# Performance work log

Hardware: AMD Instinct MI355X
Metric: run time of the kernel (lower is better)

## Reference

```python
import jax, jax.numpy as jnp
import numpy as np
import math

D_MODEL = 1024
N_HEADS = 16
HEAD_DIM = D_MODEL // N_HEADS
B, T = 2, 2048


def _rope(q, k):
    # q, k: (B, H, T, Dh)
    Dh = q.shape[-1]
    Tq = q.shape[2]
    dim = jnp.arange(0, Dh, 2, dtype=jnp.float32)
    inv_freq = 1.0 / (10000.0 ** (dim / Dh))
    pos = jnp.arange(Tq, dtype=jnp.float32)
    freqs = pos[:, None] * inv_freq[None, :]          # (T, Dh/2)
    sin = jnp.sin(freqs)[None, None]                  # (1,1,T,Dh/2)
    cos = jnp.cos(freqs)[None, None]

    def rot(t):
        te, to = t[..., ::2], t[..., 1::2]
        re = te * cos - to * sin
        ro = te * sin + to * cos
        return jnp.stack([re, ro], axis=-1).reshape(t.shape)

    return rot(q), rot(k)


def setup_inputs() -> dict:
    key = jax.random.key(0)
    ks = jax.random.split(key, 4)
    std = 1.0 / math.sqrt(D_MODEL)
    x = jax.random.normal(ks[0], (B, T, D_MODEL), dtype=jnp.float32)
    W_qkv = jax.random.normal(ks[1], (D_MODEL, 3 * D_MODEL), dtype=jnp.float32) * std
    b_qkv = jnp.zeros((3 * D_MODEL,), dtype=jnp.float32)
    W_out = jax.random.normal(ks[2], (D_MODEL, D_MODEL), dtype=jnp.float32) * std
    b_out = jnp.zeros((D_MODEL,), dtype=jnp.float32)
    attention_mask = jnp.ones((B, T), dtype=jnp.int32)
    return {"x": x, "attention_mask": attention_mask, "W_qkv": W_qkv,
            "b_qkv": b_qkv, "W_out": W_out, "b_out": b_out}


def reference(x, attention_mask, W_qkv, b_qkv, W_out, b_out):
    Bx, Tx, D = x.shape
    qkv = x @ W_qkv + b_qkv                            # (B,T,3D)
    q, k, v = jnp.split(qkv, 3, axis=-1)
    # (B,T,H,Dh) -> (B,H,T,Dh)
    q = q.reshape(Bx, Tx, N_HEADS, HEAD_DIM).transpose(0, 2, 1, 3)
    k = k.reshape(Bx, Tx, N_HEADS, HEAD_DIM).transpose(0, 2, 1, 3)
    v = v.reshape(Bx, Tx, N_HEADS, HEAD_DIM).transpose(0, 2, 1, 3)
    q, k = _rope(q, k)
    scale = 1.0 / math.sqrt(float(HEAD_DIM))
    scores = jnp.einsum('bhqd,bhkd->bhqk', q, k) * scale
    causal = jnp.tril(jnp.ones((Tx, Tx), dtype=bool))[None, None]
    pad = attention_mask.astype(bool)[:, None, None, :]
    mask = causal & pad
    scores = jnp.where(mask, scores, -jnp.inf)
    probs = jax.nn.softmax(scores, axis=-1)
    out = jnp.einsum('bhqk,bhkd->bhqd', probs, v)      # (B,H,T,Dh)
    out = out.transpose(0, 2, 1, 3).reshape(Bx, Tx, D)
    return out @ W_out + b_out
```

## Files before the change

kernel.cpp:

```cpp
#include <hip/hip_runtime.h>
#include <math.h>
#include <stdint.h>

#define D_MODEL 1024
#define N_HEADS 16
#define HEAD_DIM 64
#define BATCH 2
#define SEQ 2048
#define TOKENS (BATCH * SEQ)

typedef __attribute__((ext_vector_type(8))) short short8;
typedef __attribute__((ext_vector_type(8))) _Float16 half8;
typedef __attribute__((ext_vector_type(4))) float floatx4;

#define BMFMA(a, b, c) __builtin_amdgcn_mfma_f32_16x16x32_bf16(a, b, c, 0, 0, 0)
#define HMFMA(a, b, c) __builtin_amdgcn_mfma_f32_16x16x32_f16(a, b, c, 0, 0, 0)

__device__ __forceinline__ unsigned short f2bf(float f) {
    uint32_t u = __float_as_uint(f);
    u += 0x7fffu + ((u >> 16) & 1u);
    return (unsigned short)(u >> 16);
}
__device__ __forceinline__ float bf2f(unsigned short h) {
    return __uint_as_float(((uint32_t)h) << 16);
}
__device__ __forceinline__ unsigned short f2h(float f) {
    union { _Float16 h; unsigned short u; } cv;
    cv.h = (_Float16)f;
    return cv.u;
}
__device__ __forceinline__ float h2f(unsigned short u) {
    union { unsigned short u; _Float16 h; } cv;
    cv.u = u;
    return (float)cv.h;
}

#define GLD_LDS16(gp, lp) __builtin_amdgcn_global_load_lds(                 \
    (const __attribute__((address_space(1))) void*)(gp),                    \
    (__attribute__((address_space(3))) void*)(lp), 16, 0, 0)

__global__ __launch_bounds__(256) void split_inputs(
    const float* __restrict__ X, const float* __restrict__ Wqkv,
    const float* __restrict__ Wout, const int* __restrict__ am,
    unsigned short* __restrict__ Axh, unsigned short* __restrict__ Bt,
    unsigned short* __restrict__ Bt2, unsigned long long* __restrict__ mbits,
    float2* __restrict__ tab)
{
    __shared__ float t[32][33];
    const int tid = threadIdx.x;
    const int bid = blockIdx.x;
    if (bid < 4096) {
        const int idx = bid * 256 + tid;
        const int row = idx >> 8;
        const int c = (idx & 255) * 4;
        float4 v = *(const float4*)(X + (size_t)row * 1024 + c);
        float f[4] = {v.x, v.y, v.z, v.w};
        uint32_t hp[2], lp[2];
#pragma unroll
        for (int j = 0; j < 2; ++j) {
            unsigned short h0 = f2h(f[2 * j]), h1 = f2h(f[2 * j + 1]);
            hp[j] = (uint32_t)h0 | ((uint32_t)h1 << 16);
            lp[j] = (uint32_t)f2h(f[2 * j] - h2f(h0)) |
                    ((uint32_t)f2h(f[2 * j + 1] - h2f(h1)) << 16);
        }
        *(uint2*)(Axh + (size_t)row * 2048 + c) = make_uint2(hp[0], hp[1]);
        *(uint2*)(Axh + (size_t)row * 2048 + 1024 + c) = make_uint2(lp[0], lp[1]);
    } else if (bid < 7168) {
        const int id = bid - 4096;
        const int n0 = (id % 96) * 32, k0 = (id / 96) * 32;
        const int c = tid & 31, r = tid >> 5;
#pragma unroll
        for (int i = 0; i < 4; ++i)
            t[r + 8 * i][c] = Wqkv[(size_t)(k0 + r + 8 * i) * 3072 + n0 + c];
        __syncthreads();
#pragma unroll
        for (int i = 0; i < 4; ++i) {
            int dn = r + 8 * i;
            Bt[(size_t)(n0 + dn) * 1024 + k0 + c] = f2h(t[c][dn]);
        }
    } else if (bid < 8192) {
        const int id = bid - 7168;
        const int n0 = (id & 31) * 32, k0 = (id >> 5) * 32;
        const int c = tid & 31, r = tid >> 5;
#pragma unroll
        for (int i = 0; i < 4; ++i)
            t[r + 8 * i][c] = Wout[(size_t)(k0 + r + 8 * i) * 1024 + n0 + c];
        __syncthreads();
#pragma unroll
        for (int i = 0; i < 4; ++i) {
            int dn = r + 8 * i;
            Bt2[(size_t)(n0 + dn) * 1024 + k0 + c] = f2bf(t[c][dn]);
        }
    } else if (bid == 8192) {
        if (tid < 64) {
            const int* a = am + tid * 64;
            unsigned long long m = 0ull;
            for (int j = 0; j < 64; ++j)
                m |= (unsigned long long)(a[j] != 0 ? 1u : 0u) << j;
            mbits[tid] = m;
        }
    } else {
        const int i = bid - 8193;
#pragma unroll
        for (int e = 0; e < 16; ++e) {
            int idx = i * 4096 + e * 256 + tid;
            int tt = idx >> 5, pr = idx & 31;
            double ex = (double)(2 * pr) / 64.0;
            float inv = (float)exp2(-ex * 13.287712379549449);
            float ang = (float)tt * inv;
            float s, c;
            __sincosf(ang, &s, &c);
            tab[idx] = make_float2(c, s);
        }
    }
}

__global__ __launch_bounds__(256) void gemm_qkv_f16(
    const unsigned short* __restrict__ Axh, const unsigned short* __restrict__ Bt,
    const float* __restrict__ bias, float* __restrict__ C)
{
    __shared__ __align__(16) unsigned short sAh0[4096], sAh1[4096];
    __shared__ __align__(16) unsigned short sAl0[4096], sAl1[4096];
    __shared__ __align__(16) unsigned short sB0[4096],  sB1[4096];

    const int tid = threadIdx.x;
    const int w = tid >> 6, lane = tid & 63;
    const int l15 = lane & 15, quad = lane >> 4;
    const int wm = w >> 1, wn = w & 1;

    const bool qk = blockIdx.x < 512;
    const int lin = qk ? blockIdx.x : blockIdx.x - 512;
    const int nT = qk ? 16 : 8;
    const int msuper = lin / (8 * nT);
    const int rem = lin % (8 * nT);
    const int m0 = (msuper * 8 + (rem & 7)) * 128;
    const int n0 = (qk ? 0 : 2048) + (rem >> 3) * 128;

    const int ch = (lane & 3) ^ ((lane >> 3) & 3);
    const int sw = (quad ^ ((l15 >> 1) & 3)) * 8;

    const unsigned short* aG[2];
    const unsigned short* bG[2];
#pragma unroll
    for (int i = 0; i < 2; ++i) {
        aG[i] = Axh + (size_t)(m0 + (w * 2 + i) * 16 + (lane >> 2)) * 2048
                    + ch * 8;
        bG[i] = Bt + (size_t)(n0 + (w * 2 + i) * 16 + (lane >> 2)) * 1024
                   + ch * 8;
    }

    floatx4 acc[4][4];
#pragma unroll
    for (int fm = 0; fm < 4; ++fm)
#pragma unroll
        for (int fn = 0; fn < 4; ++fn) acc[fm][fn] = (floatx4)0.f;

    for (int ks = 0; ks < 16; ++ks) {
        const int ko = ks * 64;
        __syncthreads();
#pragma unroll
        for (int i = 0; i < 2; ++i) {
            GLD_LDS16(aG[i] + ko,        sAh0 + (w * 2 + i) * 512);
            GLD_LDS16(aG[i] + ko + 32,   sAh1 + (w * 2 + i) * 512);
            GLD_LDS16(bG[i] + ko,        sB0 + (w * 2 + i) * 512);
            GLD_LDS16(bG[i] + ko + 32,   sB1 + (w * 2 + i) * 512);
        }
        if (qk) {
#pragma unroll
            for (int i = 0; i < 2; ++i) {
                GLD_LDS16(aG[i] + 1024 + ko,      sAl0 + (w * 2 + i) * 512);
                GLD_LDS16(aG[i] + 1024 + ko + 32, sAl1 + (w * 2 + i) * 512);
            }
        }
        __syncthreads();

        half8 b0[4], b1[4];
#pragma unroll
        for (int fn = 0; fn < 4; ++fn) {
            const int off = ((wn * 4 + fn) * 16 + l15) * 32 + sw;
            b0[fn] = *(const half8*)&sB0[off];
            b1[fn] = *(const half8*)&sB1[off];
        }
#pragma unroll
        for (int fm = 0; fm < 4; ++fm) {
            const int off = ((wm * 4 + fm) * 16 + l15) * 32 + sw;
            half8 a0 = *(const half8*)&sAh0[off];
            half8 a1 = *(const half8*)&sAh1[off];
#pragma unroll
            for (int fn = 0; fn < 4; ++fn) {
                floatx4 a = acc[fm][fn];
                a = HMFMA(a0, b0[fn], a);
                a = HMFMA(a1, b1[fn], a);
                acc[fm][fn] = a;
            }
        }
        if (qk) {
#pragma unroll
            for (int fm = 0; fm < 4; ++fm) {
                const int off = ((wm * 4 + fm) * 16 + l15) * 32 + sw;
                half8 a0 = *(const half8*)&sAl0[off];
                half8 a1 = *(const half8*)&sAl1[off];
#pragma unroll
                for (int fn = 0; fn < 4; ++fn) {
                    floatx4 a = acc[fm][fn];
                    a = HMFMA(a0, b0[fn], a);
                    a = HMFMA(a1, b1[fn], a);
                    acc[fm][fn] = a;
                }
            }
        }
    }

#pragma unroll
    for (int fm = 0; fm < 4; ++fm)
#pragma unroll
        for (int fn = 0; fn < 4; ++fn) {
            int col = n0 + (wn * 4 + fn) * 16 + l15;
            float bv = bias[col];
#pragma unroll
            for (int r = 0; r < 4; ++r) {
                int row = m0 + (wm * 4 + fm) * 16 + quad * 4 + r;
                C[(size_t)row * 3072 + col] = acc[fm][fn][r] + bv;
            }
        }
}

template<int WM, int WN, int FM, int FN>
__global__ __launch_bounds__(256) void gemm_mfma_s(
    const unsigned short* __restrict__ A, int lda,
    const unsigned short* __restrict__ Bt, int ldb,
    const float* __restrict__ bias, float* __restrict__ C, int ldc, int nTiles)
{
    constexpr int BM = WM * FM * 16;
    constexpr int BN = WN * FN * 16;
    constexpr int NA = BM / 64;
    constexpr int NB = BN / 64;

    __shared__ __align__(16) unsigned short sA0[BM * 32];
    __shared__ __align__(16) unsigned short sA1[BM * 32];
    __shared__ __align__(16) unsigned short sB0[BN * 32];
    __shared__ __align__(16) unsigned short sB1[BN * 32];

    const int tid = threadIdx.x;
    const int w = tid >> 6, lane = tid & 63;
    const int l15 = lane & 15, quad = lane >> 4;
    const int wm = w / WN, wn = w % WN;

    const int lin = blockIdx.x;
    const int msuper = lin / (8 * nTiles);
    const int rem = lin % (8 * nTiles);
    const int m0 = (msuper * 8 + (rem & 7)) * BM;
    const int n0 = (rem >> 3) * BN;

    const int ch = (lane & 3) ^ ((lane >> 3) & 3);
    const int sw = (quad ^ ((l15 >> 1) & 3)) * 8;

    const unsigned short* aG[NA];
    const unsigned short* bG[NB];
#pragma unroll
    for (int i = 0; i < NA; ++i)
        aG[i] = A + (size_t)(m0 + (w * NA + i) * 16 + (lane >> 2)) * lda + ch * 8;
#pragma unroll
    for (int i = 0; i < NB; ++i)
        bG[i] = Bt + (size_t)(n0 + (w * NB + i) * 16 + (lane >> 2)) * ldb + ch * 8;

    floatx4 acc[FM][FN];
#pragma unroll
    for (int fm = 0; fm < FM; ++fm)
#pragma unroll
        for (int fn = 0; fn < FN; ++fn) acc[fm][fn] = (floatx4)0.f;

    for (int ks = 0; ks < 16; ++ks) {
        const int ko = ks * 64;
        __syncthreads();
#pragma unroll
        for (int i = 0; i < NA; ++i) {
            GLD_LDS16(aG[i] + ko,      sA0 + (w * NA + i) * 512);
            GLD_LDS16(aG[i] + ko + 32, sA1 + (w * NA + i) * 512);
        }
#pragma unroll
        for (int i = 0; i < NB; ++i) {
            GLD_LDS16(bG[i] + ko,      sB0 + (w * NB + i) * 512);
            GLD_LDS16(bG[i] + ko + 32, sB1 + (w * NB + i) * 512);
        }
        __syncthreads();

        short8 a0[FM], a1[FM], b0[FN], b1[FN];
#pragma unroll
        for (int fm = 0; fm < FM; ++fm) {
            const int off = ((wm * FM + fm) * 16 + l15) * 32 + sw;
            a0[fm] = *(const short8*)&sA0[off];
            a1[fm] = *(const short8*)&sA1[off];
        }
#pragma unroll
        for (int fn = 0; fn < FN; ++fn) {
            const int off = ((wn * FN + fn) * 16 + l15) * 32 + sw;
            b0[fn] = *(const short8*)&sB0[off];
            b1[fn] = *(const short8*)&sB1[off];
        }
#pragma unroll
        for (int fm = 0; fm < FM; ++fm)
#pragma unroll
            for (int fn = 0; fn < FN; ++fn) {
                floatx4 a = acc[fm][fn];
                a = BMFMA(a0[fm], b0[fn], a);
                a = BMFMA(a1[fm], b1[fn], a);
                acc[fm][fn] = a;
            }
    }

#pragma unroll
    for (int fm = 0; fm < FM; ++fm)
#pragma unroll
        for (int fn = 0; fn < FN; ++fn) {
            int col = n0 + (wn * FN + fn) * 16 + l15;
            float bv = bias[col];
#pragma unroll
            for (int r = 0; r < 4; ++r) {
                int row = m0 + (wm * FM + fm) * 16 + quad * 4 + r;
                C[(size_t)row * ldc + col] = acc[fm][fn][r] + bv;
            }
        }
}

__global__ __launch_bounds__(256) void prep_qkv(
    const float* __restrict__ qkv, const float2* __restrict__ tab,
    unsigned short* __restrict__ Qh,
    unsigned short* __restrict__ Kh, unsigned short* __restrict__ Kl,
    unsigned short* __restrict__ Vh)
{
    __shared__ float vt[64][65];
    const int tid = threadIdx.x;
    const int lin = blockIdx.x;
    const int tt = lin & 31, bh = lin >> 5;
    const int b = bh >> 4, h = bh & 15;
    const int r = tid >> 2;
    const int dblk = (tid & 3) * 16;
    const int tg = tt * 64 + r;
    const size_t src = (size_t)(b * SEQ + tg) * 3072 + h * 64 + dblk;
    const size_t dst = ((size_t)bh * SEQ + tg) * 64 + dblk;

    float q[16], k[16], v[16];
#pragma unroll
    for (int i = 0; i < 4; ++i) {
        *(float4*)&q[4 * i] = *(const float4*)(qkv + src + 4 * i);
        *(float4*)&k[4 * i] = *(const float4*)(qkv + src + 1024 + 4 * i);
        *(float4*)&v[4 * i] = *(const float4*)(qkv + src + 2048 + 4 * i);
    }
    float2 cs[8];
#pragma unroll
    for (int i = 0; i < 4; ++i)
        *(float4*)&cs[2 * i] = *(const float4*)(tab + (size_t)tg * 32
                                                + (dblk >> 1) + 2 * i);
#pragma unroll
    for (int j = 0; j < 16; j += 2) {
        float c = cs[j >> 1].x, s = cs[j >> 1].y;
        float qe = q[j], qo = q[j + 1];
        q[j] = qe * c - qo * s; q[j + 1] = qe * s + qo * c;
        float ke = k[j], ko = k[j + 1];
        k[j] = ke * c - ko * s; k[j + 1] = ke * s + ko * c;
    }
    uint32_t ph[8], pl[8];
#pragma unroll
    for (int j = 0; j < 8; ++j) {
        float f0 = q[2 * j] * 0.125f, f1 = q[2 * j + 1] * 0.125f;
        ph[j] = (uint32_t)f2bf(f0) | ((uint32_t)f2bf(f1) << 16);
    }
    *(uint4*)(Qh + dst) = *(uint4*)&ph[0]; *(uint4*)(Qh + dst + 8) = *(uint4*)&ph[4];
#pragma unroll
    for (int j = 0; j < 8; ++j) {
        float f0 = k[2 * j], f1 = k[2 * j + 1];
        unsigned short h0 = f2bf(f0), h1 = f2bf(f1);
        ph[j] = (uint32_t)h0 | ((uint32_t)h1 << 16);
        pl[j] = (uint32_t)f2bf(f0 - bf2f(h0)) | ((uint32_t)f2bf(f1 - bf2f(h1)) << 16);
    }
    *(uint4*)(Kh + dst) = *(uint4*)&ph[0]; *(uint4*)(Kh + dst + 8) = *(uint4*)&ph[4];
    *(uint4*)(Kl + dst) = *(uint4*)&pl[0]; *(uint4*)(Kl + dst + 8) = *(uint4*)&pl[4];

#pragma unroll
    for (int j = 0; j < 16; ++j) vt[r][dblk + j] = v[j];
    __syncthreads();
    const int d2 = tid >> 2;
    const int tb = (tid & 3) * 16;
#pragma unroll
    for (int j = 0; j < 8; ++j) {
        float f0 = vt[tb + 2 * j][d2], f1 = vt[tb + 2 * j + 1][d2];
        ph[j] = (uint32_t)f2bf(f0) | ((uint32_t)f2bf(f1) << 16);
    }
    const size_t vdst = ((size_t)bh * 64 + d2) * SEQ + tt * 64 + tb;
    *(uint4*)(Vh + vdst) = *(uint4*)&ph[0]; *(uint4*)(Vh + vdst + 8) = *(uint4*)&ph[4];
}

__global__ __launch_bounds__(256, 4) void flash_mfma(
    const unsigned short* __restrict__ Qh,
    const unsigned short* __restrict__ Kh, const unsigned short* __restrict__ Kl,
    const unsigned short* __restrict__ Vh,
    const unsigned long long* __restrict__ mbits,
    unsigned short* __restrict__ attnx)
{
    __shared__ __align__(16) unsigned short sKh[4096];
    __shared__ __align__(16) unsigned short sKl[4096];
    __shared__ __align__(16) unsigned short sVh[4096];
    __shared__ __align__(16) unsigned short sP[4096];

    const int tid = threadIdx.x;
    const int lane = tid & 63, w = tid >> 6;
    const int l15 = lane & 15, quad = lane >> 4;
    const int lin0 = blockIdx.x;
    const int xcd = lin0 & 7, idx = lin0 >> 3;
    const int bh = xcd * 4 + (idx & 3);
    const int qt = 31 - (idx >> 2);
    const int b = bh >> 4, h = bh & 15;
    const int sw = (quad ^ ((l15 >> 1) & 3)) * 8;
    const int ch = (lane & 3) ^ ((lane >> 3) & 3);
    unsigned short* pbase = sP + w * 1024;

    short8 ones;
#pragma unroll
    for (int j = 0; j < 8; ++j) ones[j] = (short)0x3F80;

    const size_t qb = ((size_t)bh * SEQ + qt * 64 + w * 16 + l15) * 64 + quad * 8;
    const short8 qh0 = *(const short8*)(Qh + qb);
    const short8 qh1 = *(const short8*)(Qh + qb + 32);

    unsigned int mlo = 0xffffffffu, mhi = 0xffffffffu;
    if (lane < 32) {
        unsigned long long mw = mbits[b * 32 + lane];
        mlo = (unsigned int)mw;
        mhi = (unsigned int)(mw >> 32);
    }
    const bool fullmask =
        (__ballot((mlo & mhi) == 0xffffffffu) == ~0ull);

    const size_t kRow0 = ((size_t)bh * SEQ + w * 16 + (lane >> 2)) * 64 + ch * 8;
    const size_t vRow  = ((size_t)bh * 64 + w * 16 + (lane >> 2)) * SEQ + ch * 8;

    floatx4 O[4];
    floatx4 lAcc = (floatx4)0.f;
#pragma unroll
    for (int nf = 0; nf < 4; ++nf) O[nf] = (floatx4)0.f;

    const int mg = qt * 64 + w * 16 + l15;

    for (int kt = 0; kt <= qt; ++kt) {
        __syncthreads();
        {
            const size_t kg = kRow0 + (size_t)kt * 64 * 64;
            const size_t vg = vRow + kt * 64;
            GLD_LDS16(Kh + kg,      sKh + w * 512);
            GLD_LDS16(Kh + kg + 32, sKh + 2048 + w * 512);
            GLD_LDS16(Kl + kg,      sKl + w * 512);
            GLD_LDS16(Kl + kg + 32, sKl + 2048 + w * 512);
            GLD_LDS16(Vh + vg,      sVh + w * 512);
            GLD_LDS16(Vh + vg + 32, sVh + 2048 + w * 512);
        }
        __syncthreads();

        const bool diag = (kt == qt);
        unsigned int wlo = 0xffffffffu, whi = 0xffffffffu;
        if (!fullmask) {
            wlo = (unsigned int)__shfl((int)mlo, kt);
            whi = (unsigned int)__shfl((int)mhi, kt);
        }

#pragma unroll
        for (int nf = 0; nf < 4; ++nf) {
            const int base = (nf * 16 + l15) * 32 + sw;
            const short8 kh0 = *(const short8*)&sKh[base];
            const short8 kh1 = *(const short8*)&sKh[2048 + base];
            const short8 kl0 = *(const short8*)&sKl[base];
            const short8 kl1 = *(const short8*)&sKl[2048 + base];
            floatx4 s = (floatx4)0.f;
            s = BMFMA(kh0, qh0, s);
            s = BMFMA(kh1, qh1, s);
            s = BMFMA(kl0, qh0, s);
            s = BMFMA(kl1, qh1, s);

            float pv[4];
            if (fullmask && !diag) {
#pragma unroll
                for (int r = 0; r < 4; ++r)
                    pv[r] = __expf(s[r] - 16.0f);
            } else {
                const int tb = kt * 64 + nf * 16 + quad * 4;
                const unsigned int msel = (nf & 2) ? whi : wlo;
                const int p4 = (nf & 1) * 16 + quad * 4;
#pragma unroll
                for (int r = 0; r < 4; ++r) {
                    bool ok = ((msel >> (p4 + r)) & 1u) != 0u;
                    if (diag) ok = ok && (tb + r <= mg);
                    pv[r] = ok ? __expf(s[r] - 16.0f) : 0.0f;
                }
            }
            uint32_t w0, w1;
            asm("v_cvt_pk_bf16_f32 %0, %1, %2" : "=v"(w0) : "v"(pv[0]), "v"(pv[1]));
            asm("v_cvt_pk_bf16_f32 %0, %1, %2" : "=v"(w1) : "v"(pv[2]), "v"(pv[3]));
            const int pos = (((nf & 1) * 2 + (quad >> 1)) ^ ((l15 >> 1) & 3));
            *(uint2*)(pbase + (nf >> 1) * 512 + l15 * 32 + pos * 8
                      + (quad & 1) * 4) = make_uint2(w0, w1);
        }

        const short8 pf0 = *(const short8*)(pbase + l15 * 32 + sw);
        const short8 pf1 = *(const short8*)(pbase + 512 + l15 * 32 + sw);

        lAcc = BMFMA(pf0, ones, lAcc);
        lAcc = BMFMA(pf1, ones, lAcc);
#pragma unroll
        for (int nf = 0; nf < 4; ++nf) {
            const int vb = (nf * 16 + l15) * 32 + sw;
            floatx4 o = O[nf];
            o = BMFMA(pf0, *(const short8*)&sVh[vb], o);
            o = BMFMA(pf1, *(const short8*)&sVh[2048 + vb], o);
            O[nf] = o;
        }
    }

    float rl[4];
#pragma unroll
    for (int r = 0; r < 4; ++r) rl[r] = 1.0f / lAcc[r];
#pragma unroll
    for (int nf = 0; nf < 4; ++nf)
#pragma unroll
        for (int r = 0; r < 4; ++r) {
            const int tok = b * SEQ + qt * 64 + w * 16 + quad * 4 + r;
            const int col = h * 64 + nf * 16 + l15;
            attnx[(size_t)tok * 1024 + col] = f2bf(O[nf][r] * rl[r]);
        }
}

extern "C" void kernel_launch(void* const* d_in, const int* in_sizes, int n_in,
                              void* d_out, int out_size, void* d_ws, size_t ws_size,
                              hipStream_t stream)
{
    const float* x    = (const float*)d_in[0];
    const int*   am   = (const int*)d_in[1];
    const float* Wqkv = (const float*)d_in[2];
    const float* bqkv = (const float*)d_in[3];
    const float* Wout = (const float*)d_in[4];
    const float* bout = (const float*)d_in[5];
    float* out = (float*)d_out;

    char* ws = (char*)d_ws;
    unsigned short* Bt  = (unsigned short*)ws;
    unsigned short* Bt2 = (unsigned short*)(ws + 6291456);
    float2* tab = (float2*)(ws + 8388608);
    unsigned long long* mbits = (unsigned long long*)(ws + 8912896);
    float* qkv = (float*)(ws + 12582912);
    unsigned short* attnx = (unsigned short*)qkv;
    unsigned short* Qh = (unsigned short*)(ws + 62914560);
    unsigned short* Kh = (unsigned short*)(ws + 71303168);
    unsigned short* Kl = (unsigned short*)(ws + 79691776);
    unsigned short* Vh = (unsigned short*)(ws + 88080384);
    unsigned short* Axh = (unsigned short*)(ws + 96468992);

    split_inputs<<<8209, 256, 0, stream>>>(x, Wqkv, Wout, am,
                                           Axh, Bt, Bt2, mbits, tab);

    gemm_qkv_f16<<<768, 256, 0, stream>>>(Axh, Bt, bqkv, qkv);

    prep_qkv<<<1024, 256, 0, stream>>>(qkv, tab, Qh, Kh, Kl, Vh);

    flash_mfma<<<1024, 256, 0, stream>>>(Qh, Kh, Kl, Vh, mbits, attnx);

    gemm_mfma_s<2, 2, 4, 4><<<256, 256, 0, stream>>>(
        attnx, 1024, Bt2, 1024, bout, out, 1024, 8);
}
```

Measured before the change: 210.5 us.

## Drop hi/lo split precision; use single fp16 throughout QKV, attention, and output

Removes the hi/lo fp16 split of x in the QKV GEMM and the hi/lo bf16 split of K in attention, so both become single-pass fp16 MFMA. The QKV GEMM output is now stored as fp16 instead of fp32. The output projection and attention output also switch to fp16. The flash kernel's query-tile ordering is changed to interleave short and long causal tiles for balance. This halves MFMA work and memory traffic in several stages, at the cost of accuracy that may approach the tolerance limit.

```diff
diff --git a/kernel.cpp b/kernel.cpp
--- a/kernel.cpp
+++ b/kernel.cpp
@@ -33,6 +33,19 @@
     union { unsigned short u; _Float16 h; } cv;
     cv.u = u;
     return (float)cv.h;
+}
+__device__ __forceinline__ void ld16h(const unsigned short* p, float* f) {
+    uint4 u0 = *(const uint4*)p;
+    uint4 u1 = *(const uint4*)(p + 8);
+    const uint32_t* a = (const uint32_t*)&u0;
+    const uint32_t* b = (const uint32_t*)&u1;
+#pragma unroll
+    for (int j = 0; j < 4; ++j) {
+        f[2 * j]     = h2f((unsigned short)(a[j] & 0xffffu));
+        f[2 * j + 1] = h2f((unsigned short)(a[j] >> 16));
+        f[8 + 2 * j]     = h2f((unsigned short)(b[j] & 0xffffu));
+        f[8 + 2 * j + 1] = h2f((unsigned short)(b[j] >> 16));
+    }
 }
 
 #define GLD_LDS16(gp, lp) __builtin_amdgcn_global_load_lds(                 \
@@ -49,24 +62,20 @@
     __shared__ float t[32][33];
     const int tid = threadIdx.x;
     const int bid = blockIdx.x;
-    if (bid < 4096) {
-        const int idx = bid * 256 + tid;
-        const int row = idx >> 8;
-        const int c = (idx & 255) * 4;
-        float4 v = *(const float4*)(X + (size_t)row * 1024 + c);
-        float f[4] = {v.x, v.y, v.z, v.w};
-        uint32_t hp[2], lp[2];
-#pragma unroll
-        for (int j = 0; j < 2; ++j) {
-            unsigned short h0 = f2h(f[2 * j]), h1 = f2h(f[2 * j + 1]);
-            hp[j] = (uint32_t)h0 | ((uint32_t)h1 << 16);
-            lp[j] = (uint32_t)f2h(f[2 * j] - h2f(h0)) |
-                    ((uint32_t)f2h(f[2 * j + 1] - h2f(h1)) << 16);
-        }
-        *(uint2*)(Axh + (size_t)row * 2048 + c) = make_uint2(hp[0], hp[1]);
-        *(uint2*)(Axh + (size_t)row * 2048 + 1024 + c) = make_uint2(lp[0], lp[1]);
-    } else if (bid < 7168) {
-        const int id = bid - 4096;
+    if (bid < 2048) {
+        const int idx = bid * 2048 + tid * 8;
+        const int row = idx >> 10;
+        const int c = idx & 1023;
+        float4 v0 = *(const float4*)(X + (size_t)row * 1024 + c);
+        float4 v1 = *(const float4*)(X + (size_t)row * 1024 + c + 4);
+        float f[8] = {v0.x, v0.y, v0.z, v0.w, v1.x, v1.y, v1.z, v1.w};
+        uint32_t p[4];
+#pragma unroll
+        for (int j = 0; j < 4; ++j)
+            p[j] = (uint32_t)f2h(f[2 * j]) | ((uint32_t)f2h(f[2 * j + 1]) << 16);
+        *(uint4*)(Axh + (size_t)row * 1024 + c) = *(uint4*)p;
+    } else if (bid < 5120) {
+        const int id = bid - 2048;
         const int n0 = (id % 96) * 32, k0 = (id / 96) * 32;
         const int c = tid & 31, r = tid >> 5;
 #pragma unroll
@@ -78,8 +87,8 @@
             int dn = r + 8 * i;
             Bt[(size_t)(n0 + dn) * 1024 + k0 + c] = f2h(t[c][dn]);
         }
-    } else if (bid < 8192) {
-        const int id = bid - 7168;
+    } else if (bid < 6144) {
+        const int id = bid - 5120;
         const int n0 = (id & 31) * 32, k0 = (id >> 5) * 32;
         const int c = tid & 31, r = tid >> 5;
 #pragma unroll
@@ -89,9 +98,9 @@
 #pragma unroll
         for (int i = 0; i < 4; ++i) {
             int dn = r + 8 * i;
-            Bt2[(size_t)(n0 + dn) * 1024 + k0 + c] = f2bf(t[c][dn]);
-        }
-    } else if (bid == 8192) {
+            Bt2[(size_t)(n0 + dn) * 1024 + k0 + c] = f2h(t[c][dn]);
+        }
+    } else if (bid == 6144) {
         if (tid < 64) {
             const int* a = am + tid * 64;
             unsigned long long m = 0ull;
@@ -100,7 +109,7 @@
             mbits[tid] = m;
         }
     } else {
-        const int i = bid - 8193;
+        const int i = bid - 6145;
 #pragma unroll
         for (int e = 0; e < 16; ++e) {
             int idx = i * 4096 + e * 256 + tid;
@@ -115,121 +124,11 @@
     }
 }
 
-__global__ __launch_bounds__(256) void gemm_qkv_f16(
-    const unsigned short* __restrict__ Axh, const unsigned short* __restrict__ Bt,
-    const float* __restrict__ bias, float* __restrict__ C)
-{
-    __shared__ __align__(16) unsigned short sAh0[4096], sAh1[4096];
-    __shared__ __align__(16) unsigned short sAl0[4096], sAl1[4096];
-    __shared__ __align__(16) unsigned short sB0[4096],  sB1[4096];
-
-    const int tid = threadIdx.x;
-    const int w = tid >> 6, lane = tid & 63;
-    const int l15 = lane & 15, quad = lane >> 4;
-    const int wm = w >> 1, wn = w & 1;
-
-    const bool qk = blockIdx.x < 512;
-    const int lin = qk ? blockIdx.x : blockIdx.x - 512;
-    const int nT = qk ? 16 : 8;
-    const int msuper = lin / (8 * nT);
-    const int rem = lin % (8 * nT);
-    const int m0 = (msuper * 8 + (rem & 7)) * 128;
-    const int n0 = (qk ? 0 : 2048) + (rem >> 3) * 128;
-
-    const int ch = (lane & 3) ^ ((lane >> 3) & 3);
-    const int sw = (quad ^ ((l15 >> 1) & 3)) * 8;
-
-    const unsigned short* aG[2];
-    const unsigned short* bG[2];
-#pragma unroll
-    for (int i = 0; i < 2; ++i) {
-        aG[i] = Axh + (size_t)(m0 + (w * 2 + i) * 16 + (lane >> 2)) * 2048
-                    + ch * 8;
-        bG[i] = Bt + (size_t)(n0 + (w * 2 + i) * 16 + (lane >> 2)) * 1024
-                   + ch * 8;
-    }
-
-    floatx4 acc[4][4];
-#pragma unroll
-    for (int fm = 0; fm < 4; ++fm)
-#pragma unroll
-        for (int fn = 0; fn < 4; ++fn) acc[fm][fn] = (floatx4)0.f;
-
-    for (int ks = 0; ks < 16; ++ks) {
-        const int ko = ks * 64;
-        __syncthreads();
-#pragma unroll
-        for (int i = 0; i < 2; ++i) {
-            GLD_LDS16(aG[i] + ko,        sAh0 + (w * 2 + i) * 512);
-            GLD_LDS16(aG[i] + ko + 32,   sAh1 + (w * 2 + i) * 512);
-            GLD_LDS16(bG[i] + ko,        sB0 + (w * 2 + i) * 512);
-            GLD_LDS16(bG[i] + ko + 32,   sB1 + (w * 2 + i) * 512);
-        }
-        if (qk) {
-#pragma unroll
-            for (int i = 0; i < 2; ++i) {
-                GLD_LDS16(aG[i] + 1024 + ko,      sAl0 + (w * 2 + i) * 512);
-                GLD_LDS16(aG[i] + 1024 + ko + 32, sAl1 + (w * 2 + i) * 512);
-            }
-        }
-        __syncthreads();
-
-        half8 b0[4], b1[4];
-#pragma unroll
-        for (int fn = 0; fn < 4; ++fn) {
-            const int off = ((wn * 4 + fn) * 16 + l15) * 32 + sw;
-            b0[fn] = *(const half8*)&sB0[off];
-            b1[fn] = *(const half8*)&sB1[off];
-        }
-#pragma unroll
-        for (int fm = 0; fm < 4; ++fm) {
-            const int off = ((wm * 4 + fm) * 16 + l15) * 32 + sw;
-            half8 a0 = *(const half8*)&sAh0[off];
-            half8 a1 = *(const half8*)&sAh1[off];
-#pragma unroll
-            for (int fn = 0; fn < 4; ++fn) {
-                floatx4 a = acc[fm][fn];
-                a = HMFMA(a0, b0[fn], a);
-                a = HMFMA(a1, b1[fn], a);
-                acc[fm][fn] = a;
-            }
-        }
-        if (qk) {
-#pragma unroll
-            for (int fm = 0; fm < 4; ++fm) {
-                const int off = ((wm * 4 + fm) * 16 + l15) * 32 + sw;
-                half8 a0 = *(const half8*)&sAl0[off];
-                half8 a1 = *(const half8*)&sAl1[off];
-#pragma unroll
-                for (int fn = 0; fn < 4; ++fn) {
-                    floatx4 a = acc[fm][fn];
-                    a = HMFMA(a0, b0[fn], a);
-                    a = HMFMA(a1, b1[fn], a);
-                    acc[fm][fn] = a;
-                }
-            }
-        }
-    }
-
-#pragma unroll
-    for (int fm = 0; fm < 4; ++fm)
-#pragma unroll
-        for (int fn = 0; fn < 4; ++fn) {
-            int col = n0 + (wn * 4 + fn) * 16 + l15;
-            float bv = bias[col];
-#pragma unroll
-            for (int r = 0; r < 4; ++r) {
-                int row = m0 + (wm * 4 + fm) * 16 + quad * 4 + r;
-                C[(size_t)row * 3072 + col] = acc[fm][fn][r] + bv;
-            }
-        }
-}
-
-template<int WM, int WN, int FM, int FN>
-__global__ __launch_bounds__(256) void gemm_mfma_s(
+template<int WM, int WN, int FM, int FN, int OUT16>
+__global__ __launch_bounds__(256) void gemm_mfma_h(
     const unsigned short* __restrict__ A, int lda,
     const unsigned short* __restrict__ Bt, int ldb,
-    const float* __restrict__ bias, float* __restrict__ C, int ldc, int nTiles)
+    const float* __restrict__ bias, void* __restrict__ Cv, int ldc, int nTiles)
 {
     constexpr int BM = WM * FM * 16;
     constexpr int BN = WN * FN * 16;
@@ -285,26 +184,26 @@
         }
         __syncthreads();
 
-        short8 a0[FM], a1[FM], b0[FN], b1[FN];
+        half8 a0[FM], a1[FM], b0[FN], b1[FN];
 #pragma unroll
         for (int fm = 0; fm < FM; ++fm) {
             const int off = ((wm * FM + fm) * 16 + l15) * 32 + sw;
-            a0[fm] = *(const short8*)&sA0[off];
-            a1[fm] = *(const short8*)&sA1[off];
+            a0[fm] = *(const half8*)&sA0[off];
+            a1[fm] = *(const half8*)&sA1[off];
         }
 #pragma unroll
         for (int fn = 0; fn < FN; ++fn) {
             const int off = ((wn * FN + fn) * 16 + l15) * 32 + sw;
-            b0[fn] = *(const short8*)&sB0[off];
-            b1[fn] = *(const short8*)&sB1[off];
+            b0[fn] = *(const half8*)&sB0[off];
+            b1[fn] = *(const half8*)&sB1[off];
         }
 #pragma unroll
         for (int fm = 0; fm < FM; ++fm)
 #pragma unroll
             for (int fn = 0; fn < FN; ++fn) {
                 floatx4 a = acc[fm][fn];
-                a = BMFMA(a0[fm], b0[fn], a);
-                a = BMFMA(a1[fm], b1[fn], a);
+                a = HMFMA(a0[fm], b0[fn], a);
+                a = HMFMA(a1[fm], b1[fn], a);
                 acc[fm][fn] = a;
             }
     }
@@ -318,15 +217,20 @@
 #pragma unroll
             for (int r = 0; r < 4; ++r) {
                 int row = m0 + (wm * FM + fm) * 16 + quad * 4 + r;
-                C[(size_t)row * ldc + col] = acc[fm][fn][r] + bv;
+                if (OUT16) {
+                    ((unsigned short*)Cv)[(size_t)row * ldc + col] =
+                        f2h(acc[fm][fn][r] + bv);
+                } else {
+                    ((float*)Cv)[(size_t)row * ldc + col] =
+                        acc[fm][fn][r] + bv;
+                }
             }
         }
 }
 
 __global__ __launch_bounds__(256) void prep_qkv(
-    const float* __restrict__ qkv, const float2* __restrict__ tab,
-    unsigned short* __restrict__ Qh,
-    unsigned short* __restrict__ Kh, unsigned short* __restrict__ Kl,
+    const unsigned short* __restrict__ qkvh, const float2* __restrict__ tab,
+    unsigned short* __restrict__ Qh, unsigned short* __restrict__ Kh,
     unsigned short* __restrict__ Vh)
 {
     __shared__ float vt[64][65];
@@ -341,12 +245,10 @@
     const size_t dst = ((size_t)bh * SEQ + tg) * 64 + dblk;
 
     float q[16], k[16], v[16];
-#pragma unroll
-    for (int i = 0; i < 4; ++i) {
-        *(float4*)&q[4 * i] = *(const float4*)(qkv + src + 4 * i);
-        *(float4*)&k[4 * i] = *(const float4*)(qkv + src + 1024 + 4 * i);
-        *(float4*)&v[4 * i] = *(const float4*)(qkv + src + 2048 + 4 * i);
-    }
+    ld16h(qkvh + src, q);
+    ld16h(qkvh + src + 1024, k);
+    ld16h(qkvh + src + 2048, v);
+
     float2 cs[8];
 #pragma unroll
     for (int i = 0; i < 4; ++i)
@@ -360,22 +262,17 @@
         float ke = k[j], ko = k[j + 1];
         k[j] = ke * c - ko * s; k[j + 1] = ke * s + ko * c;
     }
-    uint32_t ph[8], pl[8];
+    uint32_t ph[8];
 #pragma unroll
     for (int j = 0; j < 8; ++j) {
         float f0 = q[2 * j] * 0.125f, f1 = q[2 * j + 1] * 0.125f;
-        ph[j] = (uint32_t)f2bf(f0) | ((uint32_t)f2bf(f1) << 16);
+        ph[j] = (uint32_t)f2h(f0) | ((uint32_t)f2h(f1) << 16);
     }
     *(uint4*)(Qh + dst) = *(uint4*)&ph[0]; *(uint4*)(Qh + dst + 8) = *(uint4*)&ph[4];
 #pragma unroll
-    for (int j = 0; j < 8; ++j) {
-        float f0 = k[2 * j], f1 = k[2 * j + 1];
-        unsigned short h0 = f2bf(f0), h1 = f2bf(f1);
-        ph[j] = (uint32_t)h0 | ((uint32_t)h1 << 16);
-        pl[j] = (uint32_t)f2bf(f0 - bf2f(h0)) | ((uint32_t)f2bf(f1 - bf2f(h1)) << 16);
-    }
+    for (int j = 0; j < 8; ++j)
+        ph[j] = (uint32_t)f2h(k[2 * j]) | ((uint32_t)f2h(k[2 * j + 1]) << 16);
     *(uint4*)(Kh + dst) = *(uint4*)&ph[0]; *(uint4*)(Kh + dst + 8) = *(uint4*)&ph[4];
-    *(uint4*)(Kl + dst) = *(uint4*)&pl[0]; *(uint4*)(Kl + dst + 8) = *(uint4*)&pl[4];
 
 #pragma unroll
     for (int j = 0; j < 16; ++j) vt[r][dblk + j] = v[j];
@@ -392,15 +289,13 @@
 }
 
 __global__ __launch_bounds__(256, 4) void flash_mfma(
-    const unsigned short* __restrict__ Qh,
-    const unsigned short* __restrict__ Kh, const unsigned short* __restrict__ Kl,
+    const unsigned short* __restrict__ Qh, const unsigned short* __restrict__ Kh,
     const unsigned short* __restrict__ Vh,
     const unsigned long long* __restrict__ mbits,
     unsigned short* __restrict__ attnx)
 {
-    __shared__ __align__(16) unsigned short sKh[4096];
-    __shared__ __align__(16) unsigned short sKl[4096];
-    __shared__ __align__(16) unsigned short sVh[4096];
+    __shared__ __align__(16) unsigned short sK[4096];
+    __shared__ __align__(16) unsigned short sV[4096];
     __shared__ __align__(16) unsigned short sP[4096];
 
     const int tid = threadIdx.x;
@@ -408,8 +303,9 @@
     const int l15 = lane & 15, quad = lane >> 4;
     const int lin0 = blockIdx.x;
     const int xcd = lin0 & 7, idx = lin0 >> 3;
-    const int bh = xcd * 4 + (idx & 3);
-    const int qt = 31 - (idx >> 2);
+    const int g = idx >> 2, j = idx & 3;
+    const int bh = xcd * 4 + j;
+    const int qt = (j & 1) ? (31 - g) : g;
     const int b = bh >> 4, h = bh & 15;
     const int sw = (quad ^ ((l15 >> 1) & 3)) * 8;
     const int ch = (lane & 3) ^ ((lane >> 3) & 3);
@@ -417,11 +313,11 @@
 
     short8 ones;
 #pragma unroll
-    for (int j = 0; j < 8; ++j) ones[j] = (short)0x3F80;
+    for (int jj = 0; jj < 8; ++jj) ones[jj] = (short)0x3F80;
 
     const size_t qb = ((size_t)bh * SEQ + qt * 64 + w * 16 + l15) * 64 + quad * 8;
-    const short8 qh0 = *(const short8*)(Qh + qb);
-    const short8 qh1 = *(const short8*)(Qh + qb + 32);
+    const half8 qh0 = *(const half8*)(Qh + qb);
+    const half8 qh1 = *(const half8*)(Qh + qb + 32);
 
     unsigned int mlo = 0xffffffffu, mhi = 0xffffffffu;
     if (lane < 32) {
@@ -447,12 +343,10 @@
         {
             const size_t kg = kRow0 + (size_t)kt * 64 * 64;
             const size_t vg = vRow + kt * 64;
-            GLD_LDS16(Kh + kg,      sKh + w * 512);
-            GLD_LDS16(Kh + kg + 32, sKh + 2048 + w * 512);
-            GLD_LDS16(Kl + kg,      sKl + w * 512);
-            GLD_LDS16(Kl + kg + 32, sKl + 2048 + w * 512);
-            GLD_LDS16(Vh + vg,      sVh + w * 512);
-            GLD_LDS16(Vh + vg + 32, sVh + 2048 + w * 512);
+            GLD_LDS16(Kh + kg,      sK + w * 512);
+            GLD_LDS16(Kh + kg + 32, sK + 2048 + w * 512);
+            GLD_LDS16(Vh + vg,      sV + w * 512);
+            GLD_LDS16(Vh + vg + 32, sV + 2048 + w * 512);
         }
         __syncthreads();
 
@@ -466,15 +360,11 @@
 #pragma unroll
         for (int nf = 0; nf < 4; ++nf) {
             const int base = (nf * 16 + l15) * 32 + sw;
-            const short8 kh0 = *(const short8*)&sKh[base];
-            const short8 kh1 = *(const short8*)&sKh[2048 + base];
-            const short8 kl0 = *(const short8*)&sKl[base];
-            const short8 kl1 = *(const short8*)&sKl[2048 + base];
+            const half8 k0 = *(const half8*)&sK[base];
+            const half8 k1 = *(const half8*)&sK[2048 + base];
             floatx4 s = (floatx4)0.f;
-            s = BMFMA(kh0, qh0, s);
-            s = BMFMA(kh1, qh1, s);
-            s = BMFMA(kl0, qh0, s);
-            s = BMFMA(kl1, qh1, s);
+            s = HMFMA(k0, qh0, s);
+            s = HMFMA(k1, qh1, s);
 
             float pv[4];
             if (fullmask && !diag) {
@@ -509,8 +399,8 @@
         for (int nf = 0; nf < 4; ++nf) {
             const int vb = (nf * 16 + l15) * 32 + sw;
             floatx4 o = O[nf];
-            o = BMFMA(pf0, *(const short8*)&sVh[vb], o);
-            o = BMFMA(pf1, *(const short8*)&sVh[2048 + vb], o);
+            o = BMFMA(pf0, *(const short8*)&sV[vb], o);
+            o = BMFMA(pf1, *(const short8*)&sV[2048 + vb], o);
             O[nf] = o;
         }
     }
@@ -524,7 +414,7 @@
         for (int r = 0; r < 4; ++r) {
             const int tok = b * SEQ + qt * 64 + w * 16 + quad * 4 + r;
             const int col = h * 64 + nf * 16 + l15;
-            attnx[(size_t)tok * 1024 + col] = f2bf(O[nf][r] * rl[r]);
+            attnx[(size_t)tok * 1024 + col] = f2h(O[nf][r] * rl[r]);
         }
 }
 
@@ -545,23 +435,23 @@
     unsigned short* Bt2 = (unsigned short*)(ws + 6291456);
     float2* tab = (float2*)(ws + 8388608);
     unsigned long long* mbits = (unsigned long long*)(ws + 8912896);
-    float* qkv = (float*)(ws + 12582912);
-    unsigned short* attnx = (unsigned short*)qkv;
+    unsigned short* qkvh = (unsigned short*)(ws + 12582912);
+    unsigned short* attnx = qkvh;
     unsigned short* Qh = (unsigned short*)(ws + 62914560);
     unsigned short* Kh = (unsigned short*)(ws + 71303168);
-    unsigned short* Kl = (unsigned short*)(ws + 79691776);
-    unsigned short* Vh = (unsigned short*)(ws + 88080384);
-    unsigned short* Axh = (unsigned short*)(ws + 96468992);
-
-    split_inputs<<<8209, 256, 0, stream>>>(x, Wqkv, Wout, am,
+    unsigned short* Vh = (unsigned short*)(ws + 79691776);
+    unsigned short* Axh = (unsigned short*)(ws + 88080384);
+
+    split_inputs<<<6161, 256, 0, stream>>>(x, Wqkv, Wout, am,
                                            Axh, Bt, Bt2, mbits, tab);
 
-    gemm_qkv_f16<<<768, 256, 0, stream>>>(Axh, Bt, bqkv, qkv);
-
-    prep_qkv<<<1024, 256, 0, stream>>>(qkv, tab, Qh, Kh, Kl, Vh);
-
-    flash_mfma<<<1024, 256, 0, stream>>>(Qh, Kh, Kl, Vh, mbits, attnx);
-
-    gemm_mfma_s<2, 2, 4, 4><<<256, 256, 0, stream>>>(
+    gemm_mfma_h<2, 2, 4, 4, 1><<<768, 256, 0, stream>>>(
+        Axh, 1024, Bt, 1024, bqkv, qkvh, 3072, 24);
+
+    prep_qkv<<<1024, 256, 0, stream>>>(qkvh, tab, Qh, Kh, Vh);
+
+    flash_mfma<<<1024, 256, 0, stream>>>(Qh, Kh, Vh, mbits, attnx);
+
+    gemm_mfma_h<2, 2, 4, 4, 0><<<256, 256, 0, stream>>>(
         attnx, 1024, Bt2, 1024, bout, out, 1024, 8);
 }
```

After: 193.4 us. 8.1% less time.
